# Performance work log

Measured on AMD Instinct MI355X. Metric: run time of the kernel, lower is better.

The kernel has to match this reference:

```python
import jax, jax.numpy as jnp
import numpy as np
from jax import lax

B, C, FH, FW = 2, 128, 96, 160
H, W = 384, 640
NH, NP = 4, 9
T = 0.5


def conv(x, w, b, groups=1):
    pad = w.shape[2] // 2
    y = lax.conv_general_dilated(x, w, (1, 1), [(pad, pad), (pad, pad)],
                                 dimension_numbers=('NCHW', 'OIHW', 'NCHW'),
                                 feature_group_count=groups)
    return y + b[None, :, None, None]


def lrelu(x):
    return jnp.where(x >= 0, x, 0.1 * x)


def resize(x, h, w):
    # torch F.interpolate(mode='bilinear', align_corners=False, antialias=False)
    return jax.image.resize(x, (x.shape[0], x.shape[1], h, w), method='linear', antialias=False)


def grid_sample(vals, gx, gy, align_corners):
    # vals: (N, Ch, Hv, Wv); gx, gy: (N, Ho, Wo) normalized coords in [-1, 1]
    # bilinear, padding_mode='border'
    N, Ch, Hv, Wv = vals.shape
    if align_corners:
        x = (gx + 1.0) * 0.5 * (Wv - 1)
        y = (gy + 1.0) * 0.5 * (Hv - 1)
    else:
        x = ((gx + 1.0) * Wv - 1.0) * 0.5
        y = ((gy + 1.0) * Hv - 1.0) * 0.5
    x = jnp.clip(x, 0.0, Wv - 1.0)
    y = jnp.clip(y, 0.0, Hv - 1.0)
    x0 = jnp.floor(x)
    y0 = jnp.floor(y)
    wx = (x - x0)[:, None]  # (N,1,Ho,Wo)
    wy = (y - y0)[:, None]
    x0i = x0.astype(jnp.int32)
    y0i = y0.astype(jnp.int32)
    x1i = jnp.minimum(x0i + 1, Wv - 1)
    y1i = jnp.minimum(y0i + 1, Hv - 1)
    flat = vals.reshape(N, Ch, Hv * Wv)
    gather = jax.vmap(lambda v, i: jnp.take(v, i, axis=1))  # (Ch,HW),(Ho,Wo)->(Ch,Ho,Wo)
    v00 = gather(flat, y0i * Wv + x0i)
    v01 = gather(flat, y0i * Wv + x1i)
    v10 = gather(flat, y1i * Wv + x0i)
    v11 = gather(flat, y1i * Wv + x1i)
    return (v00 * (1 - wx) * (1 - wy) + v01 * wx * (1 - wy)
            + v10 * (1 - wx) * wy + v11 * wx * wy)


def warp(feat, flow):
    b, c, h, w = feat.shape
    if flow.shape[2:] != (h, w):
        sh, sw = h / flow.shape[2], w / flow.shape[3]
        flow = resize(flow, h, w) * jnp.array([sw, sh], flow.dtype)[None, :, None, None]
    gy, gx = jnp.meshgrid(jnp.arange(h, dtype=jnp.float32),
                          jnp.arange(w, dtype=jnp.float32), indexing='ij')
    gxn = 2.0 * (gx[None] + flow[:, 0]) / max(w - 1, 1) - 1.0
    gyn = 2.0 * (gy[None] + flow[:, 1]) / max(h - 1, 1) - 1.0
    return grid_sample(feat, gxn, gyn, True)


def group_norm(x, g, b, groups=8, eps=1e-5):
    B_, C_, h, w = x.shape
    xr = x.reshape(B_, groups, C_ // groups, h, w)
    m = xr.mean(axis=(2, 3, 4), keepdims=True)
    v = xr.var(axis=(2, 3, 4), keepdims=True)
    xn = ((xr - m) * lax.rsqrt(v + eps)).reshape(B_, C_, h, w)
    return xn * g[None, :, None, None] + b[None, :, None, None]


def deform_attn(q, src, ow0, ob0, ow1, ob1, aw0, ab0, aw1, ab1, vw, vb, pw, pb):
    b, c, h, w = q.shape
    hd = c // NH
    off = conv(lrelu(conv(q, ow0, ob0, groups=NH)), ow1, ob1).reshape(b, NH, NP, 2, h, w)
    attn = conv(lrelu(conv(q, aw0, ab0, groups=NH)), aw1, ab1).reshape(b, NH, NP, h, w)
    attn = jax.nn.softmax(attn, axis=2)
    vals = conv(src, vw, vb).reshape(b * NH, hd, h, w)
    gy, gx = jnp.meshgrid(jnp.arange(h, dtype=jnp.float32),
                          jnp.arange(w, dtype=jnp.float32), indexing='ij')
    sx = gx[None, None, None] + off[:, :, :, 0]  # (b,NH,NP,h,w)
    sy = gy[None, None, None] + off[:, :, :, 1]
    gxn = (2.0 * sx / max(w - 1, 1) - 1.0).reshape(b * NH, NP * h, w)
    gyn = (2.0 * sy / max(h - 1, 1) - 1.0).reshape(b * NH, NP * h, w)
    samp = grid_sample(vals, gxn, gyn, False).reshape(b, NH, hd, NP, h, w)
    out = (samp * attn[:, :, None]).sum(axis=3).reshape(b, c, h, w)
    return conv(out, pw, pb)


def setup_inputs() -> dict:
    key = jax.random.key(0)
    ks = jax.random.split(key, 24)
    rn = lambda k, s, sc: jax.random.normal(k, s, jnp.float32) * sc
    # offset conv bias: 3x3 regular grid init (n_points=9), padded with zeros
    gs = 3
    base = []
    for dy in range(gs):
        for dx in range(gs):
            base += [dx - gs // 2, dy - gs // 2]
    ob1 = np.zeros(NH * NP * 2, np.float32)
    ob1[:len(base)] = np.asarray(base, np.float32)
    return {
        'feat1': rn(ks[0], (B, C, FH, FW), 1.0),
        'feat2': rn(ks[1], (B, C, FH, FW), 1.0),
        'flow_fwd': rn(ks[2], (B, 2, H, W), 3.0),
        'flow_bwd': rn(ks[3], (B, 2, H, W), 3.0),
        'edge1': jax.random.uniform(ks[4], (B, 1, H, W), jnp.float32),
        'edge2': jax.random.uniform(ks[5], (B, 1, H, W), jnp.float32),
        'fuse_w0': rn(ks[6], (C, 2 * C + 3, 3, 3), 0.02),
        'fuse_b0': jnp.zeros((C,), jnp.float32),
        'fuse_w1': rn(ks[7], (C, C, 3, 3), 0.02),
        'fuse_b1': jnp.zeros((C,), jnp.float32),
        'gn_g': jnp.ones((C,), jnp.float32),
        'gn_b': jnp.zeros((C,), jnp.float32),
        'off_w0': rn(ks[8], (C, C // NH, 3, 3), 0.02),
        'off_b0': jnp.zeros((C,), jnp.float32),
        'off_w1': rn(ks[9], (NH * NP * 2, C, 1, 1), 0.01),
        'off_b1': jnp.asarray(ob1),
        'aw_w0': rn(ks[10], (C, C // NH, 3, 3), 0.02),
        'aw_b0': jnp.zeros((C,), jnp.float32),
        'aw_w1': rn(ks[11], (NH * NP, C, 1, 1), 0.02),
        'aw_b1': jnp.zeros((NH * NP,), jnp.float32),
        'val_w': rn(ks[12], (C, C, 1, 1), 0.05),
        'val_b': jnp.zeros((C,), jnp.float32),
        'out_w': rn(ks[13], (C, C, 1, 1), 0.05),
        'out_b': jnp.zeros((C,), jnp.float32),
        'ffn_w0': rn(ks[14], (2 * C, C, 1, 1), 0.05),
        'ffn_b0': jnp.zeros((2 * C,), jnp.float32),
        'ffn_w1': rn(ks[15], (C, 2 * C, 1, 1), 0.05),
        'ffn_b1': jnp.zeros((C,), jnp.float32),
        'dec_w0': rn(ks[16], (64, C, 3, 3), 0.03),
        'dec_b0': jnp.zeros((64,), jnp.float32),
        'dec_w1': rn(ks[17], (32, 64, 3, 3), 0.05),
        'dec_b1': jnp.zeros((32,), jnp.float32),
        'dec_w2': rn(ks[18], (3, 32, 3, 3), 0.05),
        'dec_b2': jnp.zeros((3,), jnp.float32),
    }


def reference(feat1, feat2, flow_fwd, flow_bwd, edge1, edge2,
              fuse_w0, fuse_b0, fuse_w1, fuse_b1, gn_g, gn_b,
              off_w0, off_b0, off_w1, off_b1, aw_w0, aw_b0, aw_w1, aw_b1,
              val_w, val_b, out_w, out_b, ffn_w0, ffn_b0, ffn_w1, ffn_b1,
              dec_w0, dec_b0, dec_w1, dec_b1, dec_w2, dec_b2):
    b, c, fh, fw = feat1.shape
    h, w = edge1.shape[2], edge1.shape[3]
    f1w = warp(feat1, flow_fwd * T)
    f2w = warp(feat2, flow_bwd * (1.0 - T))
    e1 = resize(edge1, fh, fw)
    e2 = resize(edge2, fh, fw)
    tmap = jnp.full((b, 1, fh, fw), T, feat1.dtype)
    fused = jnp.concatenate([f1w, f2w, e1, e2, tmap], axis=1)
    x = lrelu(conv(lrelu(conv(fused, fuse_w0, fuse_b0)), fuse_w1, fuse_b1))
    source = f1w * (1.0 - T) + f2w * T
    x = x + deform_attn(group_norm(x, gn_g, gn_b), source,
                        off_w0, off_b0, off_w1, off_b1,
                        aw_w0, aw_b0, aw_w1, aw_b1,
                        val_w, val_b, out_w, out_b)
    x = x + conv(jax.nn.gelu(conv(x, ffn_w0, ffn_b0), approximate=False), ffn_w1, ffn_b1)
    x = resize(x, h, w)
    x = lrelu(conv(x, dec_w0, dec_b0))
    x = lrelu(conv(x, dec_w1, dec_b1))
    return jax.nn.sigmoid(conv(x, dec_w2, dec_b2))
```

## Files before the change

kernel.cpp:

```cpp
#include <hip/hip_runtime.h>

typedef _Float16 f16;
typedef _Float16 f16x8 __attribute__((ext_vector_type(8)));
typedef float f32x4 __attribute__((ext_vector_type(4)));

constexpr int Bn = 2, Cn = 128, FH = 96, FW = 160, Hh = 384, Wh = 640;
constexpr int HWl = FH * FW;
constexpr int NHd = 4, NPt = 9;

#define DEVINL __device__ __forceinline__

DEVINL f32x4 zero4() { f32x4 z; z[0] = 0.f; z[1] = 0.f; z[2] = 0.f; z[3] = 0.f; return z; }
DEVINL f16x8 zero8() {
  f16x8 z;
#pragma unroll
  for (int j = 0; j < 8; ++j) z[j] = (f16)0.f;
  return z;
}

template<int ACT> DEVINL float activ(float v) {
  if (ACT == 1) return v >= 0.f ? v : 0.1f * v;
  if (ACT == 2) return 0.5f * v * (1.f + erff(v * 0.70710678118654752f));
  if (ACT == 3) return 1.f / (1.f + expf(-v));
  return v;
}

__global__ __launch_bounds__(256) void k_wprep3(
    const float* __restrict__ w, f16* __restrict__ wf,
    int Cout, int cin_g, int cout_g, int KS, int CoF)
{
  int idx = blockIdx.x * blockDim.x + threadIdx.x;
  int total = 9 * KS * CoF * 64;
  if (idx >= total) return;
  int lane = idx & 63;
  int rest = idx >> 6;
  int cf = rest % CoF;
  int rest2 = rest / CoF;
  int ks = rest2 % KS;
  int tap = rest2 / KS;
  int co = cf * 16 + (lane & 15);
  f16x8 v = zero8();
#pragma unroll
  for (int j = 0; j < 8; ++j) {
    int kl = (lane >> 4) * 8 + j;
    int cip = ks * 32 + kl;
    int cil = cip - (co / cout_g) * cin_g;
    float x = 0.f;
    if (co < Cout && cil >= 0 && cil < cin_g)
      x = w[((size_t)co * cin_g + cil) * 9 + tap];
    v[j] = (f16)x;
  }
  *(f16x8*)&wf[(size_t)idx * 8] = v;
}

__global__ __launch_bounds__(256) void k_wprep1(
    const float* __restrict__ w, f16* __restrict__ wf,
    int Cout, int Cin, int KS, int CoF)
{
  int idx = blockIdx.x * blockDim.x + threadIdx.x;
  int total = KS * CoF * 64;
  if (idx >= total) return;
  int lane = idx & 63;
  int cf = (idx >> 6) % CoF;
  int ks = (idx >> 6) / CoF;
  int co = cf * 16 + (lane & 15);
  f16x8 v = zero8();
#pragma unroll
  for (int j = 0; j < 8; ++j) {
    int cip = ks * 32 + (lane >> 4) * 8 + j;
    float x = 0.f;
    if (co < Cout && cip < Cin) x = w[(size_t)co * Cin + cip];
    v[j] = (f16)x;
  }
  *(f16x8*)&wf[(size_t)idx * 8] = v;
}

__global__ __launch_bounds__(256) void k_warp_fuse_h(
    const float* __restrict__ feat1, const float* __restrict__ feat2,
    const float* __restrict__ flowf, const float* __restrict__ flowb,
    const float* __restrict__ edge1, const float* __restrict__ edge2,
    f16* __restrict__ fused, f16* __restrict__ src)
{
  int idx = blockIdx.x * blockDim.x + threadIdx.x;
  if (idx >= Bn * 8 * HWl) return;
  int pix = idx % HWl;
  int cq = (idx / HWl) & 7;
  int b = idx / (HWl * 8);
  int j = pix % FW;
  int i = pix / FW;

  const int y4 = 4 * i + 1, x4 = 4 * j + 1;
  const float* p;
  p = flowf + (size_t)((b * 2 + 0) * Hh + y4) * Wh + x4;
  float fx1 = 0.03125f * (p[0] + p[1] + p[Wh] + p[Wh + 1]);
  p = flowf + (size_t)((b * 2 + 1) * Hh + y4) * Wh + x4;
  float fy1 = 0.03125f * (p[0] + p[1] + p[Wh] + p[Wh + 1]);
  p = flowb + (size_t)((b * 2 + 0) * Hh + y4) * Wh + x4;
  float fx2 = 0.03125f * (p[0] + p[1] + p[Wh] + p[Wh + 1]);
  p = flowb + (size_t)((b * 2 + 1) * Hh + y4) * Wh + x4;
  float fy2 = 0.03125f * (p[0] + p[1] + p[Wh] + p[Wh + 1]);

  float sx1 = fminf(fmaxf((float)j + fx1, 0.f), (float)(FW - 1));
  float sy1 = fminf(fmaxf((float)i + fy1, 0.f), (float)(FH - 1));
  float sx2 = fminf(fmaxf((float)j + fx2, 0.f), (float)(FW - 1));
  float sy2 = fminf(fmaxf((float)i + fy2, 0.f), (float)(FH - 1));

  int x10 = (int)floorf(sx1), y10 = (int)floorf(sy1);
  int x11 = min(x10 + 1, FW - 1), y11 = min(y10 + 1, FH - 1);
  float wx1 = sx1 - (float)x10, wy1 = sy1 - (float)y10;
  int x20 = (int)floorf(sx2), y20 = (int)floorf(sy2);
  int x21 = min(x20 + 1, FW - 1), y21 = min(y20 + 1, FH - 1);
  float wx2 = sx2 - (float)x20, wy2 = sy2 - (float)y20;

  float a00 = (1.f - wx1) * (1.f - wy1), a01 = wx1 * (1.f - wy1);
  float a10 = (1.f - wx1) * wy1,         a11 = wx1 * wy1;
  float c00 = (1.f - wx2) * (1.f - wy2), c01 = wx2 * (1.f - wy2);
  float c10 = (1.f - wx2) * wy2,         c11 = wx2 * wy2;
  int o00 = y10 * FW + x10, o01 = y10 * FW + x11, o10 = y11 * FW + x10, o11 = y11 * FW + x11;
  int q00 = y20 * FW + x20, q01 = y20 * FW + x21, q10 = y21 * FW + x20, q11 = y21 * FW + x21;

  f16* fp = fused + ((size_t)b * HWl + pix) * 288;
  f16* sp = src + ((size_t)b * HWl + pix) * 128;

  if (cq == 0) {
    p = edge1 + (size_t)(b * Hh + y4) * Wh + x4;
    float e1v = 0.25f * (p[0] + p[1] + p[Wh] + p[Wh + 1]);
    p = edge2 + (size_t)(b * Hh + y4) * Wh + x4;
    float e2v = 0.25f * (p[0] + p[1] + p[Wh] + p[Wh + 1]);
    fp[256] = (f16)e1v;
    fp[257] = (f16)e2v;
    fp[258] = (f16)0.5f;
#pragma unroll
    for (int c = 259; c < 288; ++c) fp[c] = (f16)0.f;
  }

  int c0 = cq * 16;
  for (int c = c0; c < c0 + 16; ++c) {
    const float* f1 = feat1 + (size_t)(b * Cn + c) * HWl;
    const float* f2 = feat2 + (size_t)(b * Cn + c) * HWl;
    float v1 = f1[o00] * a00 + f1[o01] * a01 + f1[o10] * a10 + f1[o11] * a11;
    float v2 = f2[q00] * c00 + f2[q01] * c01 + f2[q10] * c10 + f2[q11] * c11;
    fp[c] = (f16)v1;
    fp[128 + c] = (f16)v2;
    sp[c] = (f16)(0.5f * (v1 + v2));
  }
}

template<int ACT, int UP, int NF>
__global__ __launch_bounds__(256) void k_conv3m(
    const f16* __restrict__ Xin, const f16* __restrict__ Wf,
    const float* __restrict__ bias, f16* __restrict__ Out,
    int KS, int CoF, int Cs_in, int Cs_out, int Wd, int Ht,
    int in_r0, int in_rows, int out_r0, int out_rows, int ogr0, int ogr1)
{
  __shared__ f16 sA[8160];
  int tid = threadIdx.x;
  int wv = tid >> 6, lane = tid & 63;
  int l15 = lane & 15, l4 = lane >> 4;
  int colTiles = Wd >> 5;
  int tileC = blockIdx.x % colTiles, tileR = blockIdx.x / colTiles;
  int b = blockIdx.z;
  int co0 = blockIdx.y * (NF * 16);
  int cfB = blockIdx.y * NF;
  int rowBaseOut = ogr0 + tileR * 4;
  int rowBase = rowBaseOut - 1;
  int colBase = tileC * 32;

  f32x4 acc[2][NF];
#pragma unroll
  for (int mf = 0; mf < 2; ++mf)
#pragma unroll
    for (int nf = 0; nf < NF; ++nf) acc[mf][nf] = zero4();

  for (int cs = 0; cs < KS; ++cs) {
    for (int u = tid; u < 816; u += 256) {
      int s = u & 3;
      int pxy = u >> 2;
      int x = pxy % 34;
      int y = pxy / 34;
      int gy = rowBase + y;
      int gx = colBase + x - 1;
      f16x8 v = zero8();
      if (UP) {
        if (gy >= 0 && gy < Ht && gx >= 0 && gx < Wd) {
          float uy = ((float)gy + 0.5f) * 0.25f - 0.5f;
          uy = fminf(fmaxf(uy, 0.f), (float)(FH - 1));
          int y0 = (int)floorf(uy);
          int y1 = min(y0 + 1, FH - 1);
          float fy = uy - (float)y0;
          float ux = ((float)gx + 0.5f) * 0.25f - 0.5f;
          ux = fminf(fmaxf(ux, 0.f), (float)(FW - 1));
          int x0 = (int)floorf(ux);
          int x1 = min(x0 + 1, FW - 1);
          float fx = ux - (float)x0;
          const f16* xb = Xin + (size_t)b * HWl * 128 + cs * 32 + s * 8;
          f16x8 v00 = *(const f16x8*)&xb[(size_t)(y0 * FW + x0) * 128];
          f16x8 v01 = *(const f16x8*)&xb[(size_t)(y0 * FW + x1) * 128];
          f16x8 v10 = *(const f16x8*)&xb[(size_t)(y1 * FW + x0) * 128];
          f16x8 v11 = *(const f16x8*)&xb[(size_t)(y1 * FW + x1) * 128];
#pragma unroll
          for (int jj = 0; jj < 8; ++jj) {
            float t0 = (float)v00[jj] * (1.f - fx) + (float)v01[jj] * fx;
            float t1 = (float)v10[jj] * (1.f - fx) + (float)v11[jj] * fx;
            v[jj] = (f16)(t0 * (1.f - fy) + t1 * fy);
          }
        }
      } else {
        if (gy >= in_r0 && gy < in_r0 + in_rows && gx >= 0 && gx < Wd)
          v = *(const f16x8*)&Xin[(((size_t)b * in_rows + (gy - in_r0)) * Wd + gx) * Cs_in
                                  + cs * 32 + s * 8];
      }
      *(f16x8*)((char*)sA + pxy * 80 + s * 16) = v;
    }
    __syncthreads();
#pragma unroll
    for (int ky = 0; ky < 3; ++ky) {
#pragma unroll
      for (int kx = 0; kx < 3; ++kx) {
        const char* ab = (const char*)sA;
        f16x8 a0 = *(const f16x8*)(ab + ((wv + ky) * 34 + l15 + kx) * 80 + l4 * 16);
        f16x8 a1 = *(const f16x8*)(ab + ((wv + ky) * 34 + l15 + 16 + kx) * 80 + l4 * 16);
        int tap = ky * 3 + kx;
#pragma unroll
        for (int nf = 0; nf < NF; ++nf) {
          f16x8 bf = *(const f16x8*)&Wf[((((size_t)tap * KS + cs) * CoF + cfB + nf) * 64 + lane) * 8];
          acc[0][nf] = __builtin_amdgcn_mfma_f32_16x16x32_f16(a0, bf, acc[0][nf], 0, 0, 0);
          acc[1][nf] = __builtin_amdgcn_mfma_f32_16x16x32_f16(a1, bf, acc[1][nf], 0, 0, 0);
        }
      }
    }
    __syncthreads();
  }

  int r = rowBaseOut + wv;
  if (r < ogr1) {
    size_t rowoff = ((size_t)b * out_rows + (r - out_r0)) * Wd;
#pragma unroll
    for (int nf = 0; nf < NF; ++nf) {
      int co = co0 + nf * 16 + l15;
      float bv = bias[co];
#pragma unroll
      for (int mf = 0; mf < 2; ++mf) {
        int xo = colBase + mf * 16 + l4 * 4;
#pragma unroll
        for (int rg = 0; rg < 4; ++rg) {
          float v = activ<ACT>(acc[mf][nf][rg] + bv);
          Out[(rowoff + xo + rg) * Cs_out + co] = (f16)v;
        }
      }
    }
  }
}

template<int ACT, int RES>
__global__ __launch_bounds__(256) void k_gemm1x1(
    const f16* __restrict__ X, const f16* __restrict__ Wf,
    const float* __restrict__ bias, f16* __restrict__ Out,
    int KS, int CoF, int Cs_in, int Cs_out, int Cr, int coTiles, int pixTiles)
{
  int wid = blockIdx.x * 4 + (threadIdx.x >> 6);
  int lane = threadIdx.x & 63;
  int total = pixTiles * coTiles;
  if (wid >= total) return;
  int coT = wid % coTiles;
  int pixT = wid / coTiles;
  int nfc = min(4, CoF - coT * 4);
  int l15 = lane & 15, l4 = lane >> 4;

  f32x4 acc[2][4];
#pragma unroll
  for (int mf = 0; mf < 2; ++mf)
#pragma unroll
    for (int nf = 0; nf < 4; ++nf) acc[mf][nf] = zero4();

  int pA0 = pixT * 32 + l15;
  for (int ks = 0; ks < KS; ++ks) {
    f16x8 a0 = *(const f16x8*)&X[(size_t)pA0 * Cs_in + ks * 32 + l4 * 8];
    f16x8 a1 = *(const f16x8*)&X[(size_t)(pA0 + 16) * Cs_in + ks * 32 + l4 * 8];
#pragma unroll
    for (int nf = 0; nf < 4; ++nf) {
      if (nf < nfc) {
        f16x8 bf = *(const f16x8*)&Wf[(((size_t)ks * CoF + coT * 4 + nf) * 64 + lane) * 8];
        acc[0][nf] = __builtin_amdgcn_mfma_f32_16x16x32_f16(a0, bf, acc[0][nf], 0, 0, 0);
        acc[1][nf] = __builtin_amdgcn_mfma_f32_16x16x32_f16(a1, bf, acc[1][nf], 0, 0, 0);
      }
    }
  }
#pragma unroll
  for (int nf = 0; nf < 4; ++nf) {
    if (nf < nfc) {
      int co = coT * 64 + nf * 16 + l15;
      if (co < Cr) {
        float bv = bias[co];
#pragma unroll
        for (int mf = 0; mf < 2; ++mf) {
          int p0 = pixT * 32 + mf * 16 + l4 * 4;
#pragma unroll
          for (int rg = 0; rg < 4; ++rg) {
            float v = activ<ACT>(acc[mf][nf][rg] + bv);
            size_t o = (size_t)(p0 + rg) * Cs_out + co;
            if (RES) v += (float)Out[o];
            Out[o] = (f16)v;
          }
        }
      }
    }
  }
}

__global__ __launch_bounds__(256) void k_gn_part_h(
    const f16* __restrict__ X, float* __restrict__ part)
{
  int s = blockIdx.x & 7;
  int g = (blockIdx.x >> 3) & 7;
  int b = blockIdx.x >> 6;
  int tid = threadIdx.x;
  const f16* Xp = X + (size_t)b * HWl * 128 + g * 16 + (tid & 1) * 8;
  float sum = 0.f, ss = 0.f;
  for (int p = s * 1920 + (tid >> 1); p < (s + 1) * 1920; p += 128) {
    f16x8 v = *(const f16x8*)&Xp[(size_t)p * 128];
#pragma unroll
    for (int jj = 0; jj < 8; ++jj) { float f = (float)v[jj]; sum += f; ss += f * f; }
  }
  __shared__ float sh1[256], sh2[256];
  sh1[tid] = sum; sh2[tid] = ss;
  __syncthreads();
  for (int st = 128; st > 0; st >>= 1) {
    if (tid < st) { sh1[tid] += sh1[tid + st]; sh2[tid] += sh2[tid + st]; }
    __syncthreads();
  }
  if (tid == 0) {
    part[((b * 8 + g) * 8 + s) * 2] = sh1[0];
    part[((b * 8 + g) * 8 + s) * 2 + 1] = sh2[0];
  }
}

__global__ __launch_bounds__(256) void k_gn_apply_h(
    const f16* __restrict__ X, const float* __restrict__ gw,
    const float* __restrict__ gb, const float* __restrict__ part,
    f16* __restrict__ Q)
{
  int idx = blockIdx.x * blockDim.x + threadIdx.x;
  int total = Bn * HWl * 16;
  if (idx >= total) return;
  int u = idx & 15;
  int pix = (idx >> 4) % HWl;
  int b = idx / (16 * HWl);
  int c0 = u * 8;
  int g = c0 >> 4;
  const float* pp = part + ((b * 8 + g) * 8) * 2;
  float sum = 0.f, ss = 0.f;
#pragma unroll
  for (int s = 0; s < 8; ++s) { sum += pp[s * 2]; ss += pp[s * 2 + 1]; }
  const float n = 16.f * HWl;
  float mean = sum / n;
  float var = ss / n - mean * mean;
  float inv = rsqrtf(var + 1e-5f);
  f16x8 v = *(const f16x8*)&X[((size_t)b * HWl + pix) * 128 + c0];
  f16x8 r;
#pragma unroll
  for (int jj = 0; jj < 8; ++jj) {
    int c = c0 + jj;
    r[jj] = (f16)(((float)v[jj] - mean) * (gw[c] * inv) + gb[c]);
  }
  *(f16x8*)&Q[((size_t)b * HWl + pix) * 128 + c0] = r;
}

__global__ __launch_bounds__(256) void k_softmax9_h(f16* __restrict__ a)
{
  int idx = blockIdx.x * blockDim.x + threadIdx.x;
  if (idx >= Bn * NHd * HWl) return;
  int pix = idx % HWl;
  int head = (idx / HWl) & 3;
  int b = idx / (HWl * NHd);
  f16* base = a + ((size_t)b * HWl + pix) * 48 + head * 9;
  float v[9];
  float m = -1e30f;
#pragma unroll
  for (int p0 = 0; p0 < 9; ++p0) { v[p0] = (float)base[p0]; m = fmaxf(m, v[p0]); }
  float s = 0.f;
#pragma unroll
  for (int p0 = 0; p0 < 9; ++p0) { v[p0] = expf(v[p0] - m); s += v[p0]; }
  float inv = 1.f / s;
#pragma unroll
  for (int p0 = 0; p0 < 9; ++p0) base[p0] = (f16)(v[p0] * inv);
}

__global__ __launch_bounds__(256) void k_deform_h(
    const f16* __restrict__ vals, const f16* __restrict__ off,
    const f16* __restrict__ attn, f16* __restrict__ outa)
{
  int idx = blockIdx.x * blockDim.x + threadIdx.x;
  if (idx >= Bn * NHd * HWl) return;
  int pix = idx % HWl;
  int head = (idx / HWl) & 3;
  int b = idx / (HWl * NHd);
  int j = pix % FW, i = pix / FW;

  const float kx = (float)FW / (float)(FW - 1);
  const float ky = (float)FH / (float)(FH - 1);
  const f16* vb = vals + (size_t)b * HWl * 128 + head * 32;
  const f16* ab = attn + ((size_t)b * HWl + pix) * 48 + head * 9;
  const f16* ob = off + ((size_t)b * HWl + pix) * 80 + head * 18;

  float acc[32];
#pragma unroll
  for (int k = 0; k < 32; ++k) acc[k] = 0.f;

#pragma unroll
  for (int p0 = 0; p0 < 9; ++p0) {
    float ox = (float)ob[p0 * 2];
    float oy = (float)ob[p0 * 2 + 1];
    float aw = (float)ab[p0];
    float xf = ((float)j + ox) * kx - 0.5f;
    float yf = ((float)i + oy) * ky - 0.5f;
    xf = fminf(fmaxf(xf, 0.f), (float)(FW - 1));
    yf = fminf(fmaxf(yf, 0.f), (float)(FH - 1));
    int x0 = (int)floorf(xf), y0 = (int)floorf(yf);
    int x1 = min(x0 + 1, FW - 1), y1 = min(y0 + 1, FH - 1);
    float fx = xf - (float)x0, fy = yf - (float)y0;
    float w00 = aw * (1.f - fx) * (1.f - fy);
    float w01 = aw * fx * (1.f - fy);
    float w10 = aw * (1.f - fx) * fy;
    float w11 = aw * fx * fy;
    const f16x8* c00 = (const f16x8*)&vb[(size_t)(y0 * FW + x0) * 128];
    const f16x8* c01 = (const f16x8*)&vb[(size_t)(y0 * FW + x1) * 128];
    const f16x8* c10 = (const f16x8*)&vb[(size_t)(y1 * FW + x0) * 128];
    const f16x8* c11 = (const f16x8*)&vb[(size_t)(y1 * FW + x1) * 128];
#pragma unroll
    for (int k8 = 0; k8 < 4; ++k8) {
      f16x8 a = c00[k8], bb = c01[k8], cc = c10[k8], dd = c11[k8];
#pragma unroll
      for (int jj = 0; jj < 8; ++jj)
        acc[k8 * 8 + jj] += w00 * (float)a[jj] + w01 * (float)bb[jj]
                          + w10 * (float)cc[jj] + w11 * (float)dd[jj];
    }
  }
  f16* op = outa + ((size_t)b * HWl + pix) * 128 + head * 32;
#pragma unroll
  for (int k = 0; k < 32; ++k) op[k] = (f16)acc[k];
}

__global__ __launch_bounds__(256) void k_dec2_h(
    const f16* __restrict__ Xb, const float* __restrict__ w,
    const float* __restrict__ bias, float* __restrict__ out,
    int c0, int b0, int brows)
{
  int idx = blockIdx.x * blockDim.x + threadIdx.x;
  if (idx >= Bn * 96 * Wh) return;
  int x = idx % Wh;
  int y = c0 + (idx / Wh) % 96;
  int b = idx / (Wh * 96);
  float a0 = bias[0], a1 = bias[1], a2 = bias[2];
#pragma unroll
  for (int ky = 0; ky < 3; ++ky) {
    int gy = y + ky - 1;
    if (gy < 0 || gy >= Hh) continue;
#pragma unroll
    for (int kxx = 0; kxx < 3; ++kxx) {
      int gx = x + kxx - 1;
      if (gx < 0 || gx >= Wh) continue;
      int tap = ky * 3 + kxx;
      const f16* px = Xb + ((size_t)(b * brows + (gy - b0)) * Wh + gx) * 32;
#pragma unroll
      for (int k8 = 0; k8 < 4; ++k8) {
        f16x8 v = *(const f16x8*)&px[k8 * 8];
#pragma unroll
        for (int jj = 0; jj < 8; ++jj) {
          int ci = k8 * 8 + jj;
          float f = (float)v[jj];
          a0 += f * w[(0 * 32 + ci) * 9 + tap];
          a1 += f * w[(1 * 32 + ci) * 9 + tap];
          a2 += f * w[(2 * 32 + ci) * 9 + tap];
        }
      }
    }
  }
  size_t o = ((size_t)(b * 3 + 0) * Hh + y) * Wh + x;
  out[o] = 1.f / (1.f + expf(-a0));
  out[o + (size_t)Hh * Wh] = 1.f / (1.f + expf(-a1));
  out[o + (size_t)2 * Hh * Wh] = 1.f / (1.f + expf(-a2));
}

extern "C" void kernel_launch(void* const* d_in, const int* in_sizes, int n_in,
                              void* d_out, int out_size, void* d_ws, size_t ws_size,
                              hipStream_t stream) {
  (void)in_sizes; (void)n_in; (void)out_size; (void)ws_size;
  const float* feat1  = (const float*)d_in[0];
  const float* feat2  = (const float*)d_in[1];
  const float* flowf  = (const float*)d_in[2];
  const float* flowb  = (const float*)d_in[3];
  const float* edge1  = (const float*)d_in[4];
  const float* edge2  = (const float*)d_in[5];
  const float* fuse_w0 = (const float*)d_in[6];
  const float* fuse_b0 = (const float*)d_in[7];
  const float* fuse_w1 = (const float*)d_in[8];
  const float* fuse_b1 = (const float*)d_in[9];
  const float* gn_g   = (const float*)d_in[10];
  const float* gn_b   = (const float*)d_in[11];
  const float* off_w0 = (const float*)d_in[12];
  const float* off_b0 = (const float*)d_in[13];
  const float* off_w1 = (const float*)d_in[14];
  const float* off_b1 = (const float*)d_in[15];
  const float* aw_w0  = (const float*)d_in[16];
  const float* aw_b0  = (const float*)d_in[17];
  const float* aw_w1  = (const float*)d_in[18];
  const float* aw_b1  = (const float*)d_in[19];
  const float* val_w  = (const float*)d_in[20];
  const float* val_b  = (const float*)d_in[21];
  const float* out_w  = (const float*)d_in[22];
  const float* out_b  = (const float*)d_in[23];
  const float* ffn_w0 = (const float*)d_in[24];
  const float* ffn_b0 = (const float*)d_in[25];
  const float* ffn_w1 = (const float*)d_in[26];
  const float* ffn_b1 = (const float*)d_in[27];
  const float* dec_w0 = (const float*)d_in[28];
  const float* dec_b0 = (const float*)d_in[29];
  const float* dec_w1 = (const float*)d_in[30];
  const float* dec_b1 = (const float*)d_in[31];
  const float* dec_w2 = (const float*)d_in[32];
  const float* dec_b2 = (const float*)d_in[33];
  float* out = (float*)d_out;

  f16* ws16 = (f16*)d_ws;
  size_t o = 0;
  auto alloc = [&](size_t n) { f16* p = ws16 + o; o += (n + 7) & ~(size_t)7; return p; };
  f16* xbuf  = alloc((size_t)2 * HWl * 128);
  f16* regA  = alloc((size_t)2 * HWl * 288);
  f16* regB  = alloc((size_t)2 * HWl * 128);
  f16* regC  = alloc((size_t)2 * HWl * 128);
  f16* offb  = alloc((size_t)2 * HWl * 80);
  f16* attnb = alloc((size_t)2 * HWl * 48);
  f16* regF  = alloc((size_t)2 * 98 * 640 * 32);
  f16* wfF0 = alloc(9 * 288 * 128);
  f16* wfF1 = alloc(9 * 128 * 128);
  f16* wfO0 = alloc(9 * 128 * 128);
  f16* wfA0 = alloc(9 * 128 * 128);
  f16* wfD0 = alloc(9 * 128 * 64);
  f16* wfD1 = alloc(9 * 64 * 32);
  f16* w1O  = alloc(4 * 5 * 512);
  f16* w1A  = alloc(4 * 3 * 512);
  f16* w1V  = alloc(4 * 8 * 512);
  f16* w1U  = alloc(4 * 8 * 512);
  f16* w1G0 = alloc(4 * 16 * 512);
  f16* w1G1 = alloc(8 * 8 * 512);
  float* gnp = (float*)alloc(512);

  f16* fused = regA;
  f16* t_off = regA;
  f16* t_aw  = regA;
  f16* ffn_t = regA;
  f16* bufA  = regA;
  f16* src_h = regB;
  f16* out_attn = regB;
  f16* tmp_h = regC;
  f16* qb    = regC;
  f16* valsb = regF;
  f16* bufB  = regF;

  dim3 blk(256);
  auto pg = [](long n) { return dim3((unsigned)((n + 255) / 256)); };

  k_wprep3<<<pg(9L * 9 * 8 * 64), blk, 0, stream>>>(fuse_w0, wfF0, 128, 259, 128, 9, 8);
  k_wprep3<<<pg(9L * 4 * 8 * 64), blk, 0, stream>>>(fuse_w1, wfF1, 128, 128, 128, 4, 8);
  k_wprep3<<<pg(9L * 4 * 8 * 64), blk, 0, stream>>>(off_w0, wfO0, 128, 32, 32, 4, 8);
  k_wprep3<<<pg(9L * 4 * 8 * 64), blk, 0, stream>>>(aw_w0, wfA0, 128, 32, 32, 4, 8);
  k_wprep3<<<pg(9L * 4 * 4 * 64), blk, 0, stream>>>(dec_w0, wfD0, 64, 128, 64, 4, 4);
  k_wprep3<<<pg(9L * 2 * 2 * 64), blk, 0, stream>>>(dec_w1, wfD1, 32, 64, 32, 2, 2);
  k_wprep1<<<pg(4L * 5 * 64), blk, 0, stream>>>(off_w1, w1O, 72, 128, 4, 5);
  k_wprep1<<<pg(4L * 3 * 64), blk, 0, stream>>>(aw_w1, w1A, 36, 128, 4, 3);
  k_wprep1<<<pg(4L * 8 * 64), blk, 0, stream>>>(val_w, w1V, 128, 128, 4, 8);
  k_wprep1<<<pg(4L * 8 * 64), blk, 0, stream>>>(out_w, w1U, 128, 128, 4, 8);
  k_wprep1<<<pg(4L * 16 * 64), blk, 0, stream>>>(ffn_w0, w1G0, 256, 128, 4, 16);
  k_wprep1<<<pg(8L * 8 * 64), blk, 0, stream>>>(ffn_w1, w1G1, 128, 256, 8, 8);

  k_warp_fuse_h<<<pg(2L * 8 * HWl), blk, 0, stream>>>(feat1, feat2, flowf, flowb,
                                                      edge1, edge2, fused, src_h);
  dim3 gF(24 * 5, 2, 2);
  k_conv3m<1, 0, 4><<<gF, blk, 0, stream>>>(fused, wfF0, fuse_b0, tmp_h,
      9, 8, 288, 128, FW, FH, 0, FH, 0, FH, 0, FH);
  k_conv3m<1, 0, 4><<<gF, blk, 0, stream>>>(tmp_h, wfF1, fuse_b1, xbuf,
      4, 8, 128, 128, FW, FH, 0, FH, 0, FH, 0, FH);
  k_gn_part_h<<<dim3(128), blk, 0, stream>>>(xbuf, gnp);
  k_gn_apply_h<<<pg(2L * HWl * 16), blk, 0, stream>>>(xbuf, gn_g, gn_b, gnp, qb);
  k_conv3m<1, 0, 4><<<gF, blk, 0, stream>>>(qb, wfO0, off_b0, t_off,
      4, 8, 128, 128, FW, FH, 0, FH, 0, FH, 0, FH);
  k_gemm1x1<0, 0><<<dim3(480), blk, 0, stream>>>(t_off, w1O, off_b1, offb,
      4, 5, 128, 80, 72, 2, 960);
  k_conv3m<1, 0, 4><<<gF, blk, 0, stream>>>(qb, wfA0, aw_b0, t_aw,
      4, 8, 128, 128, FW, FH, 0, FH, 0, FH, 0, FH);
  k_gemm1x1<0, 0><<<dim3(240), blk, 0, stream>>>(t_aw, w1A, aw_b1, attnb,
      4, 3, 128, 48, 36, 1, 960);
  k_softmax9_h<<<pg(2L * NHd * HWl), blk, 0, stream>>>(attnb);
  k_gemm1x1<0, 0><<<dim3(480), blk, 0, stream>>>(src_h, w1V, val_b, valsb,
      4, 8, 128, 128, 128, 2, 960);
  k_deform_h<<<pg(2L * NHd * HWl), blk, 0, stream>>>(valsb, offb, attnb, out_attn);
  k_gemm1x1<0, 1><<<dim3(480), blk, 0, stream>>>(out_attn, w1U, out_b, xbuf,
      4, 8, 128, 128, 128, 2, 960);
  k_gemm1x1<2, 0><<<dim3(960), blk, 0, stream>>>(xbuf, w1G0, ffn_b0, ffn_t,
      4, 16, 128, 256, 256, 4, 960);
  k_gemm1x1<0, 1><<<dim3(480), blk, 0, stream>>>(ffn_t, w1G1, ffn_b1, xbuf,
      8, 8, 256, 128, 128, 2, 960);

  for (int c0 = 0; c0 < Hh; c0 += 96) {
    int c1 = c0 + 96;
    int a0 = c0 - 2 > 0 ? c0 - 2 : 0;
    int a1 = c1 + 2 < Hh ? c1 + 2 : Hh;
    int b0 = c0 - 1 > 0 ? c0 - 1 : 0;
    int b1 = c1 + 1 < Hh ? c1 + 1 : Hh;
    int ar = a1 - a0, br = b1 - b0;
    dim3 gD0((unsigned)(((ar + 3) / 4) * 20), 1, 2);
    k_conv3m<1, 1, 4><<<gD0, blk, 0, stream>>>(xbuf, wfD0, dec_b0, bufA,
        4, 4, 128, 64, Wh, Hh, 0, 0, a0, ar, a0, a1);
    dim3 gD1((unsigned)(((br + 3) / 4) * 20), 1, 2);
    k_conv3m<1, 0, 2><<<gD1, blk, 0, stream>>>(bufA, wfD1, dec_b1, bufB,
        2, 2, 64, 32, Wh, Hh, a0, ar, b0, br, b0, b1);
    k_dec2_h<<<pg(2L * 96 * Wh), blk, 0, stream>>>(bufB, dec_w2, dec_b2, out, c0, b0, br);
  }
}
```

Before: 625.0 us.

## Merge weight prep, transpose features for warp, prefetch conv tiles, larger decoder chunks

```diff
diff --git a/kernel.cpp b/kernel.cpp
--- a/kernel.cpp
+++ b/kernel.cpp
@@ -25,67 +25,73 @@
   return v;
 }
 
-__global__ __launch_bounds__(256) void k_wprep3(
-    const float* __restrict__ w, f16* __restrict__ wf,
-    int Cout, int cin_g, int cout_g, int KS, int CoF)
-{
-  int idx = blockIdx.x * blockDim.x + threadIdx.x;
-  int total = 9 * KS * CoF * 64;
+struct PrepJob { const float* w; f16* wf; int Cout, cin_g, cout_g, KS, CoF, taps, blk0; };
+struct PrepArgs { PrepJob j[12]; };
+
+__global__ __launch_bounds__(256) void k_wprep_all(PrepArgs a)
+{
+  int jb = 0;
+#pragma unroll
+  for (int t = 1; t < 12; ++t) if ((int)blockIdx.x >= a.j[t].blk0) jb = t;
+  PrepJob J = a.j[jb];
+  int idx = (blockIdx.x - J.blk0) * 256 + threadIdx.x;
+  int total = J.taps * J.KS * J.CoF * 64;
   if (idx >= total) return;
   int lane = idx & 63;
   int rest = idx >> 6;
-  int cf = rest % CoF;
-  int rest2 = rest / CoF;
-  int ks = rest2 % KS;
-  int tap = rest2 / KS;
+  int cf = rest % J.CoF;
+  int rest2 = rest / J.CoF;
+  int ks = rest2 % J.KS;
+  int tap = rest2 / J.KS;
   int co = cf * 16 + (lane & 15);
   f16x8 v = zero8();
 #pragma unroll
   for (int j = 0; j < 8; ++j) {
-    int kl = (lane >> 4) * 8 + j;
-    int cip = ks * 32 + kl;
-    int cil = cip - (co / cout_g) * cin_g;
+    int cip = ks * 32 + (lane >> 4) * 8 + j;
+    int cil = cip - (co / J.cout_g) * J.cin_g;
     float x = 0.f;
-    if (co < Cout && cil >= 0 && cil < cin_g)
-      x = w[((size_t)co * cin_g + cil) * 9 + tap];
+    if (co < J.Cout && cil >= 0 && cil < J.cin_g)
+      x = J.w[((size_t)co * J.cin_g + cil) * J.taps + tap];
     v[j] = (f16)x;
   }
-  *(f16x8*)&wf[(size_t)idx * 8] = v;
-}
-
-__global__ __launch_bounds__(256) void k_wprep1(
-    const float* __restrict__ w, f16* __restrict__ wf,
-    int Cout, int Cin, int KS, int CoF)
+  *(f16x8*)&J.wf[(size_t)idx * 8] = v;
+}
+
+__global__ __launch_bounds__(256) void k_tr_h(
+    const float* __restrict__ feat1, const float* __restrict__ feat2,
+    f16* __restrict__ t1, f16* __restrict__ t2)
 {
   int idx = blockIdx.x * blockDim.x + threadIdx.x;
-  int total = KS * CoF * 64;
-  if (idx >= total) return;
-  int lane = idx & 63;
-  int cf = (idx >> 6) % CoF;
-  int ks = (idx >> 6) / CoF;
-  int co = cf * 16 + (lane & 15);
-  f16x8 v = zero8();
+  if (idx >= 2 * Bn * HWl * 8) return;
+  int cq = idx & 7;
+  int pix = (idx >> 3) % HWl;
+  int z = idx / (8 * HWl);
+  int b = z & 1;
+  const float* src = (z >> 1) ? feat2 : feat1;
+  f16* dst = (z >> 1) ? t2 : t1;
+  int c0 = cq * 16;
+  f16x8 v0, v1;
 #pragma unroll
   for (int j = 0; j < 8; ++j) {
-    int cip = ks * 32 + (lane >> 4) * 8 + j;
-    float x = 0.f;
-    if (co < Cout && cip < Cin) x = w[(size_t)co * Cin + cip];
-    v[j] = (f16)x;
-  }
-  *(f16x8*)&wf[(size_t)idx * 8] = v;
+    v0[j] = (f16)src[(size_t)(b * Cn + c0 + j) * HWl + pix];
+    v1[j] = (f16)src[(size_t)(b * Cn + c0 + 8 + j) * HWl + pix];
+  }
+  f16* dp = dst + ((size_t)b * HWl + pix) * 128 + c0;
+  *(f16x8*)dp = v0;
+  *(f16x8*)(dp + 8) = v1;
 }
 
 __global__ __launch_bounds__(256) void k_warp_fuse_h(
-    const float* __restrict__ feat1, const float* __restrict__ feat2,
+    const f16* __restrict__ t1, const f16* __restrict__ t2,
     const float* __restrict__ flowf, const float* __restrict__ flowb,
     const float* __restrict__ edge1, const float* __restrict__ edge2,
     f16* __restrict__ fused, f16* __restrict__ src)
 {
   int idx = blockIdx.x * blockDim.x + threadIdx.x;
-  if (idx >= Bn * 8 * HWl) return;
-  int pix = idx % HWl;
-  int cq = (idx / HWl) & 7;
-  int b = idx / (HWl * 8);
+  if (idx >= Bn * HWl * 8) return;
+  int cq = idx & 7;
+  int pix = (idx >> 3) % HWl;
+  int b = idx / (8 * HWl);
   int j = pix % FW;
   int i = pix / FW;
 
@@ -116,11 +122,39 @@
   float a10 = (1.f - wx1) * wy1,         a11 = wx1 * wy1;
   float c00 = (1.f - wx2) * (1.f - wy2), c01 = wx2 * (1.f - wy2);
   float c10 = (1.f - wx2) * wy2,         c11 = wx2 * wy2;
-  int o00 = y10 * FW + x10, o01 = y10 * FW + x11, o10 = y11 * FW + x10, o11 = y11 * FW + x11;
-  int q00 = y20 * FW + x20, q01 = y20 * FW + x21, q10 = y21 * FW + x20, q11 = y21 * FW + x21;
+
+  int c0 = cq * 16;
+  const f16* b1 = t1 + (size_t)b * HWl * 128 + c0;
+  const f16* b2 = t2 + (size_t)b * HWl * 128 + c0;
+  const f16x8* p100 = (const f16x8*)&b1[(size_t)(y10 * FW + x10) * 128];
+  const f16x8* p101 = (const f16x8*)&b1[(size_t)(y10 * FW + x11) * 128];
+  const f16x8* p110 = (const f16x8*)&b1[(size_t)(y11 * FW + x10) * 128];
+  const f16x8* p111 = (const f16x8*)&b1[(size_t)(y11 * FW + x11) * 128];
+  const f16x8* p200 = (const f16x8*)&b2[(size_t)(y20 * FW + x20) * 128];
+  const f16x8* p201 = (const f16x8*)&b2[(size_t)(y20 * FW + x21) * 128];
+  const f16x8* p210 = (const f16x8*)&b2[(size_t)(y21 * FW + x20) * 128];
+  const f16x8* p211 = (const f16x8*)&b2[(size_t)(y21 * FW + x21) * 128];
 
   f16* fp = fused + ((size_t)b * HWl + pix) * 288;
   f16* sp = src + ((size_t)b * HWl + pix) * 128;
+
+#pragma unroll
+  for (int h = 0; h < 2; ++h) {
+    f16x8 u00 = p100[h], u01 = p101[h], u10 = p110[h], u11 = p111[h];
+    f16x8 w00 = p200[h], w01 = p201[h], w10 = p210[h], w11 = p211[h];
+    f16x8 r1, r2, rs;
+#pragma unroll
+    for (int k = 0; k < 8; ++k) {
+      float v1 = (float)u00[k] * a00 + (float)u01[k] * a01
+               + (float)u10[k] * a10 + (float)u11[k] * a11;
+      float v2 = (float)w00[k] * c00 + (float)w01[k] * c01
+               + (float)w10[k] * c10 + (float)w11[k] * c11;
+      r1[k] = (f16)v1; r2[k] = (f16)v2; rs[k] = (f16)(0.5f * (v1 + v2));
+    }
+    *(f16x8*)(fp + c0 + h * 8) = r1;
+    *(f16x8*)(fp + 128 + c0 + h * 8) = r2;
+    *(f16x8*)(sp + c0 + h * 8) = rs;
+  }
 
   if (cq == 0) {
     p = edge1 + (size_t)(b * Hh + y4) * Wh + x4;
@@ -132,17 +166,6 @@
     fp[258] = (f16)0.5f;
 #pragma unroll
     for (int c = 259; c < 288; ++c) fp[c] = (f16)0.f;
-  }
-
-  int c0 = cq * 16;
-  for (int c = c0; c < c0 + 16; ++c) {
-    const float* f1 = feat1 + (size_t)(b * Cn + c) * HWl;
-    const float* f2 = feat2 + (size_t)(b * Cn + c) * HWl;
-    float v1 = f1[o00] * a00 + f1[o01] * a01 + f1[o10] * a10 + f1[o11] * a11;
-    float v2 = f2[q00] * c00 + f2[q01] * c01 + f2[q10] * c10 + f2[q11] * c11;
-    fp[c] = (f16)v1;
-    fp[128 + c] = (f16)v2;
-    sp[c] = (f16)(0.5f * (v1 + v2));
   }
 }
 
@@ -172,47 +195,82 @@
 #pragma unroll
     for (int nf = 0; nf < NF; ++nf) acc[mf][nf] = zero4();
 
-  for (int cs = 0; cs < KS; ++cs) {
-    for (int u = tid; u < 816; u += 256) {
-      int s = u & 3;
-      int pxy = u >> 2;
-      int x = pxy % 34;
-      int y = pxy / 34;
-      int gy = rowBase + y;
-      int gx = colBase + x - 1;
-      f16x8 v = zero8();
-      if (UP) {
-        if (gy >= 0 && gy < Ht && gx >= 0 && gx < Wd) {
+  f16x8 stv[4];
+  f16x8 stc[4][4];
+
+  auto prefetch = [&](int cs) {
+#pragma unroll
+    for (int k = 0; k < 4; ++k) {
+      int u = tid + k * 256;
+      if (u < 816) {
+        int s = u & 3;
+        int pxy = u >> 2;
+        int x = pxy % 34, y = pxy / 34;
+        int gy = rowBase + y, gx = colBase + x - 1;
+        if (UP) {
+          stc[k][0] = zero8(); stc[k][1] = zero8();
+          stc[k][2] = zero8(); stc[k][3] = zero8();
+          if (gy >= 0 && gy < Ht && gx >= 0 && gx < Wd) {
+            float uy = ((float)gy + 0.5f) * 0.25f - 0.5f;
+            uy = fminf(fmaxf(uy, 0.f), (float)(FH - 1));
+            int y0 = (int)floorf(uy);
+            int y1 = min(y0 + 1, FH - 1);
+            float ux = ((float)gx + 0.5f) * 0.25f - 0.5f;
+            ux = fminf(fmaxf(ux, 0.f), (float)(FW - 1));
+            int x0 = (int)floorf(ux);
+            int x1 = min(x0 + 1, FW - 1);
+            const f16* xb = Xin + (size_t)b * HWl * 128 + cs * 32 + s * 8;
+            stc[k][0] = *(const f16x8*)&xb[(size_t)(y0 * FW + x0) * 128];
+            stc[k][1] = *(const f16x8*)&xb[(size_t)(y0 * FW + x1) * 128];
+            stc[k][2] = *(const f16x8*)&xb[(size_t)(y1 * FW + x0) * 128];
+            stc[k][3] = *(const f16x8*)&xb[(size_t)(y1 * FW + x1) * 128];
+          }
+        } else {
+          stv[k] = zero8();
+          if (gy >= in_r0 && gy < in_r0 + in_rows && gx >= 0 && gx < Wd)
+            stv[k] = *(const f16x8*)&Xin[(((size_t)b * in_rows + (gy - in_r0)) * Wd + gx) * Cs_in
+                                         + cs * 32 + s * 8];
+        }
+      }
+    }
+  };
+
+  auto writeLDS = [&]() {
+#pragma unroll
+    for (int k = 0; k < 4; ++k) {
+      int u = tid + k * 256;
+      if (u < 816) {
+        int s = u & 3;
+        int pxy = u >> 2;
+        f16x8 v;
+        if (UP) {
+          int x = pxy % 34, y = pxy / 34;
+          int gy = rowBase + y, gx = colBase + x - 1;
           float uy = ((float)gy + 0.5f) * 0.25f - 0.5f;
           uy = fminf(fmaxf(uy, 0.f), (float)(FH - 1));
-          int y0 = (int)floorf(uy);
-          int y1 = min(y0 + 1, FH - 1);
-          float fy = uy - (float)y0;
+          float fy = uy - floorf(uy);
           float ux = ((float)gx + 0.5f) * 0.25f - 0.5f;
           ux = fminf(fmaxf(ux, 0.f), (float)(FW - 1));
-          int x0 = (int)floorf(ux);
-          int x1 = min(x0 + 1, FW - 1);
-          float fx = ux - (float)x0;
-          const f16* xb = Xin + (size_t)b * HWl * 128 + cs * 32 + s * 8;
-          f16x8 v00 = *(const f16x8*)&xb[(size_t)(y0 * FW + x0) * 128];
-          f16x8 v01 = *(const f16x8*)&xb[(size_t)(y0 * FW + x1) * 128];
-          f16x8 v10 = *(const f16x8*)&xb[(size_t)(y1 * FW + x0) * 128];
-          f16x8 v11 = *(const f16x8*)&xb[(size_t)(y1 * FW + x1) * 128];
+          float fx = ux - floorf(ux);
 #pragma unroll
           for (int jj = 0; jj < 8; ++jj) {
-            float t0 = (float)v00[jj] * (1.f - fx) + (float)v01[jj] * fx;
-            float t1 = (float)v10[jj] * (1.f - fx) + (float)v11[jj] * fx;
+            float t0 = (float)stc[k][0][jj] * (1.f - fx) + (float)stc[k][1][jj] * fx;
+            float t1 = (float)stc[k][2][jj] * (1.f - fx) + (float)stc[k][3][jj] * fx;
             v[jj] = (f16)(t0 * (1.f - fy) + t1 * fy);
           }
+        } else {
+          v = stv[k];
         }
-      } else {
-        if (gy >= in_r0 && gy < in_r0 + in_rows && gx >= 0 && gx < Wd)
-          v = *(const f16x8*)&Xin[(((size_t)b * in_rows + (gy - in_r0)) * Wd + gx) * Cs_in
-                                  + cs * 32 + s * 8];
+        *(f16x8*)((char*)sA + pxy * 80 + s * 16) = v;
       }
-      *(f16x8*)((char*)sA + pxy * 80 + s * 16) = v;
-    }
+    }
+  };
+
+  prefetch(0);
+  for (int cs = 0; cs < KS; ++cs) {
+    writeLDS();
     __syncthreads();
+    if (cs + 1 < KS) prefetch(cs + 1);
 #pragma unroll
     for (int ky = 0; ky < 3; ++ky) {
 #pragma unroll
@@ -444,13 +502,13 @@
 __global__ __launch_bounds__(256) void k_dec2_h(
     const f16* __restrict__ Xb, const float* __restrict__ w,
     const float* __restrict__ bias, float* __restrict__ out,
-    int c0, int b0, int brows)
+    int c0, int b0, int brows, int R)
 {
   int idx = blockIdx.x * blockDim.x + threadIdx.x;
-  if (idx >= Bn * 96 * Wh) return;
+  if (idx >= Bn * R * Wh) return;
   int x = idx % Wh;
-  int y = c0 + (idx / Wh) % 96;
-  int b = idx / (Wh * 96);
+  int y = c0 + (idx / Wh) % R;
+  int b = idx / (Wh * R);
   float a0 = bias[0], a1 = bias[1], a2 = bias[2];
 #pragma unroll
   for (int ky = 0; ky < 3; ++ky) {
@@ -526,12 +584,15 @@
   size_t o = 0;
   auto alloc = [&](size_t n) { f16* p = ws16 + o; o += (n + 7) & ~(size_t)7; return p; };
   f16* xbuf  = alloc((size_t)2 * HWl * 128);
+  f16* pool  = alloc((size_t)0);
   f16* regA  = alloc((size_t)2 * HWl * 288);
   f16* regB  = alloc((size_t)2 * HWl * 128);
   f16* regC  = alloc((size_t)2 * HWl * 128);
   f16* offb  = alloc((size_t)2 * HWl * 80);
   f16* attnb = alloc((size_t)2 * HWl * 48);
-  f16* regF  = alloc((size_t)2 * 98 * 640 * 32);
+  f16* regF  = alloc((size_t)2 * HWl * 131);
+  f16* featT1 = alloc((size_t)2 * HWl * 128);
+  f16* featT2 = alloc((size_t)2 * HWl * 128);
   f16* wfF0 = alloc(9 * 288 * 128);
   f16* wfF1 = alloc(9 * 128 * 128);
   f16* wfO0 = alloc(9 * 128 * 128);
@@ -550,32 +611,47 @@
   f16* t_off = regA;
   f16* t_aw  = regA;
   f16* ffn_t = regA;
-  f16* bufA  = regA;
   f16* src_h = regB;
   f16* out_attn = regB;
   f16* tmp_h = regC;
   f16* qb    = regC;
   f16* valsb = regF;
-  f16* bufB  = regF;
+  f16* bufA  = pool;
+  f16* bufB  = pool + (size_t)2 * 196 * 640 * 64;
 
   dim3 blk(256);
   auto pg = [](long n) { return dim3((unsigned)((n + 255) / 256)); };
 
-  k_wprep3<<<pg(9L * 9 * 8 * 64), blk, 0, stream>>>(fuse_w0, wfF0, 128, 259, 128, 9, 8);
-  k_wprep3<<<pg(9L * 4 * 8 * 64), blk, 0, stream>>>(fuse_w1, wfF1, 128, 128, 128, 4, 8);
-  k_wprep3<<<pg(9L * 4 * 8 * 64), blk, 0, stream>>>(off_w0, wfO0, 128, 32, 32, 4, 8);
-  k_wprep3<<<pg(9L * 4 * 8 * 64), blk, 0, stream>>>(aw_w0, wfA0, 128, 32, 32, 4, 8);
-  k_wprep3<<<pg(9L * 4 * 4 * 64), blk, 0, stream>>>(dec_w0, wfD0, 64, 128, 64, 4, 4);
-  k_wprep3<<<pg(9L * 2 * 2 * 64), blk, 0, stream>>>(dec_w1, wfD1, 32, 64, 32, 2, 2);
-  k_wprep1<<<pg(4L * 5 * 64), blk, 0, stream>>>(off_w1, w1O, 72, 128, 4, 5);
-  k_wprep1<<<pg(4L * 3 * 64), blk, 0, stream>>>(aw_w1, w1A, 36, 128, 4, 3);
-  k_wprep1<<<pg(4L * 8 * 64), blk, 0, stream>>>(val_w, w1V, 128, 128, 4, 8);
-  k_wprep1<<<pg(4L * 8 * 64), blk, 0, stream>>>(out_w, w1U, 128, 128, 4, 8);
-  k_wprep1<<<pg(4L * 16 * 64), blk, 0, stream>>>(ffn_w0, w1G0, 256, 128, 4, 16);
-  k_wprep1<<<pg(8L * 8 * 64), blk, 0, stream>>>(ffn_w1, w1G1, 128, 256, 8, 8);
-
-  k_warp_fuse_h<<<pg(2L * 8 * HWl), blk, 0, stream>>>(feat1, feat2, flowf, flowb,
-                                                      edge1, edge2, fused, src_h);
+  PrepArgs pa;
+  int pb = 0;
+  auto addj = [&](int k, const float* w, f16* wf, int Cout, int cing, int coutg,
+                  int KS, int CoF, int taps) {
+    pa.j[k] = PrepJob{w, wf, Cout, cing, coutg, KS, CoF, taps, pb};
+    pb += (taps * KS * CoF * 64 + 255) / 256;
+  };
+  addj(0, fuse_w0, wfF0, 128, 259, 128, 9, 8, 9);
+  addj(1, fuse_w1, wfF1, 128, 128, 128, 4, 8, 9);
+  addj(2, off_w0, wfO0, 128, 32, 32, 4, 8, 9);
+  addj(3, aw_w0,  wfA0, 128, 32, 32, 4, 8, 9);
+  addj(4, dec_w0, wfD0, 64, 128, 64, 4, 4, 9);
+  addj(5, dec_w1, wfD1, 32, 64, 32, 2, 2, 9);
+  addj(6, off_w1, w1O, 72, 128, 128, 4, 5, 1);
+  addj(7, aw_w1,  w1A, 36, 128, 128, 4, 3, 1);
+  addj(8, val_w,  w1V, 128, 128, 128, 4, 8, 1);
+  addj(9, out_w,  w1U, 128, 128, 128, 4, 8, 1);
+  addj(10, ffn_w0, w1G0, 256, 128, 128, 4, 16, 1);
+  addj(11, ffn_w1, w1G1, 128, 256, 256, 8, 8, 1);
+  pa.j[6].cin_g = 128;  pa.j[6].cout_g = 72;
+  pa.j[7].cin_g = 128;  pa.j[7].cout_g = 36;
+  pa.j[8].cin_g = 128;  pa.j[8].cout_g = 128;
+  pa.j[9].cin_g = 128;  pa.j[9].cout_g = 128;
+  pa.j[10].cin_g = 128; pa.j[10].cout_g = 256;
+  pa.j[11].cin_g = 256; pa.j[11].cout_g = 128;
+  k_wprep_all<<<dim3((unsigned)pb), blk, 0, stream>>>(pa);
+
+  k_tr_h<<<pg(2L * Bn * HWl * 8), blk, 0, stream>>>(feat1, feat2, featT1, featT2);
+  k_warp_fuse_h<<<pg((long)Bn * HWl * 8), blk, 0, stream>>>(featT1, featT2, flowf, flowb,
+                                                            edge1, edge2, fused, src_h);
   dim3 gF(24 * 5, 2, 2);
   k_conv3m<1, 0, 4><<<gF, blk, 0, stream>>>(fused, wfF0, fuse_b0, tmp_h,
       9, 8, 288, 128, FW, FH, 0, FH, 0, FH, 0, FH);
@@ -602,8 +678,8 @@
   k_gemm1x1<0, 1><<<dim3(480), blk, 0, stream>>>(ffn_t, w1G1, ffn_b1, xbuf,
       8, 8, 256, 128, 128, 2, 960);
 
-  for (int c0 = 0; c0 < Hh; c0 += 96) {
-    int c1 = c0 + 96;
+  for (int c0 = 0; c0 < Hh; c0 += 192) {
+    int c1 = c0 + 192;
     int a0 = c0 - 2 > 0 ? c0 - 2 : 0;
     int a1 = c1 + 2 < Hh ? c1 + 2 : Hh;
     int b0 = c0 - 1 > 0 ? c0 - 1 : 0;
@@ -615,6 +691,7 @@
     dim3 gD1((unsigned)(((br + 3) / 4) * 20), 1, 2);
     k_conv3m<1, 0, 2><<<gD1, blk, 0, stream>>>(bufA, wfD1, dec_b1, bufB,
         2, 2, 64, 32, Wh, Hh, a0, ar, b0, br, b0, b1);
-    k_dec2_h<<<pg(2L * 96 * Wh), blk, 0, stream>>>(bufB, dec_w2, dec_b2, out, c0, b0, br);
-  }
-}
+    k_dec2_h<<<pg(2L * 192 * Wh), blk, 0, stream>>>(bufB, dec_w2, dec_b2, out,
+                                                    c0, b0, br, 192);
+  }
+}
```

Measured after the change: 610.5 us. -2.3%, faster.
